# Kernel tuning notes

Hardware: AMD Instinct MI355X
Metric: run time of the kernel (lower is better)

## Reference

```python
import jax, jax.numpy as jnp
import numpy as np

MAX_GROUPS = 8
NUM_DIRECTIONS = 7
NEG = -1e9


def setup_inputs() -> dict:
    key = jax.random.key(0)
    ks = jax.random.split(key, 8)
    num_nodes, B, D = 262144, 4096, 128
    node_features = jax.random.normal(ks[0], (num_nodes, D), dtype=jnp.float32)
    global_features = jax.random.normal(ks[1], (B, D), dtype=jnp.float32)
    group_mask = jax.random.bernoulli(ks[2], 0.2, (num_nodes,))
    maneuver_valid_mask = jax.random.bernoulli(ks[3], 0.5, (B, MAX_GROUPS * NUM_DIRECTIONS))
    batch = jnp.sort(jax.random.randint(ks[4], (num_nodes,), 0, B)).astype(jnp.int32)
    w1 = jax.random.normal(ks[5], (2 * D, 128), dtype=jnp.float32) * 0.05
    b1 = jnp.zeros((128,), dtype=jnp.float32)
    w2 = jax.random.normal(ks[6], (128, NUM_DIRECTIONS), dtype=jnp.float32) * 0.05
    b2 = jnp.zeros((NUM_DIRECTIONS,), dtype=jnp.float32)
    return {"node_features": node_features, "global_features": global_features,
            "group_mask": group_mask, "maneuver_valid_mask": maneuver_valid_mask,
            "batch": batch, "w1": w1, "b1": b1, "w2": w2, "b2": b2}


def reference(node_features, global_features, group_mask, maneuver_valid_mask, batch, w1, b1, w2, b2):
    B, Dg = global_features.shape
    N, D = node_features.shape
    G, R = MAX_GROUPS, NUM_DIRECTIONS
    gm = group_mask.astype(jnp.int32)
    # batch is sorted, so within-batch group order == global node order.
    counts = jax.ops.segment_sum(gm, batch, num_segments=B)            # groups per graph
    base = jnp.concatenate([jnp.zeros((1,), jnp.int32), jnp.cumsum(counts)])[:-1]
    rank = jnp.cumsum(gm) - 1 - base[batch]                            # within-batch group index
    valid = group_mask & (rank < G)
    slot = jnp.where(valid, batch * G + rank, B * G)                   # dummy row B*G for dropped nodes
    feats = jnp.zeros((B * G + 1, D), node_features.dtype).at[slot].set(node_features)
    occ = jnp.zeros((B * G + 1,), bool).at[slot].set(valid)
    feats = feats[:-1].reshape(B, G, D)
    occ = occ[:-1].reshape(B, G)
    x = jnp.concatenate([feats, jnp.broadcast_to(global_features[:, None, :], (B, G, Dg))], axis=-1)
    h = jax.nn.relu(jnp.einsum('bgd,dk->bgk', x, w1) + b1)
    scores = jnp.einsum('bgk,kr->bgr', h, w2) + b2                     # [B, G, R]
    logits = jnp.where(occ[:, :, None], scores, NEG).reshape(B, G * R)
    return jnp.where(maneuver_valid_mask, logits, NEG)
```

## Files before the change

### kernel.cpp

```cpp
#include <hip/hip_runtime.h>


#define MAXG 8
#define NDIR 7
#define NEGV -1e9f

typedef __attribute__((ext_vector_type(8))) short s8v;
typedef __attribute__((ext_vector_type(4))) float f32x4;

__device__ inline bool readMask(const void* p, int i, int fmt) {
    switch (fmt) {
        case 0: return ((const int*)p)[i] != 0;
        case 1: return ((const unsigned char*)p)[i] != 0;
        case 2: return ((const float*)p)[i] != 0.0f;
        default: return ((const unsigned short*)p)[i] != 0;
    }
}

__global__ __launch_bounds__(256) void fused_all(
        const float* __restrict__ nf,
        const float* __restrict__ gf,
        const void*  __restrict__ gm,
        const void*  __restrict__ mv,
        const int*   __restrict__ batch,
        const float* __restrict__ w1,
        const float* __restrict__ b1,
        const float* __restrict__ w2,
        const float* __restrict__ b2,
        float* __restrict__ out,
        int N, int B)
{
    __shared__ int sStart[9];
    __shared__ int sSlot[64];
    __shared__ int sFlag[8];
    __shared__ __align__(16) short w1s[128 * 40];
    __shared__ __align__(16) float hT[64 * 132];

    int t = threadIdx.x;
    int b0 = blockIdx.x * 8;
    int rowBase = blockIdx.x * 64;

    if (t < 64) sSlot[t] = -1;
    if (t < 8)  sFlag[t] = 1;
    __syncthreads();

    {
        const unsigned int*   wg = (const unsigned int*)gm;
        const unsigned short* hg = (const unsigned short*)gm;
        const unsigned int*   wm = (const unsigned int*)mv;
        const unsigned short* hm = (const unsigned short*)mv;
        int oW=1,oH=1,oHf=1,oEv=1, pW=1,pH=1,pHf=1,pEv=1;
        for (int i = t; i < 1024; i += 256) {
            if (wg[i] > 1u) oW = 0;
            if (wm[i] > 1u) pW = 0;
        }
        for (int i = t; i < 2048; i += 256) {
            unsigned short v = hg[i];
            if (v && v != 0x3F80) oH = 0;
            if (v && v != 0x3C00) oHf = 0;
            if (!(i & 1) && v) oEv = 0;
            unsigned short u = hm[i];
            if (u && u != 0x3F80) pH = 0;
            if (u && u != 0x3C00) pHf = 0;
            if (!(i & 1) && u) pEv = 0;
        }
        if (!oW)  atomicAnd(&sFlag[0], 0);
        if (!oH)  atomicAnd(&sFlag[1], 0);
        if (!oHf) atomicAnd(&sFlag[2], 0);
        if (!oEv) atomicAnd(&sFlag[3], 0);
        if (!pW)  atomicAnd(&sFlag[4], 0);
        if (!pH)  atomicAnd(&sFlag[5], 0);
        if (!pHf) atomicAnd(&sFlag[6], 0);
        if (!pEv) atomicAnd(&sFlag[7], 0);
    }

    if (t < 9) {
        int target = b0 + t;
        int lo = 0, hi = N;
        while (lo < hi) {
            int mid = (lo + hi) >> 1;
            if (batch[mid] < target) lo = mid + 1; else hi = mid;
        }
        sStart[t] = lo;
    }
    __syncthreads();

    int fmtG, fmtM;
    if (sFlag[0]) fmtG = 0; else if (sFlag[1]) fmtG = sFlag[3] ? 2 : 3;
    else if (sFlag[2]) fmtG = 4; else fmtG = 1;
    if (sFlag[4]) fmtM = 0; else if (sFlag[5]) fmtM = sFlag[7] ? 2 : 3;
    else if (sFlag[6]) fmtM = 4; else fmtM = 1;

    int wave = t >> 6, lane = t & 63;
    for (int sub = 0; sub < 2; ++sub) {
        int lb = wave * 2 + sub;
        int s = sStart[lb], e = sStart[lb + 1];
        int count = 0;
        for (int i0 = s; i0 < e && count < MAXG; i0 += 64) {
            int i = i0 + lane;
            bool m = (i < e) && readMask(gm, i, fmtG);
            unsigned long long bal = __ballot(m);
            unsigned long long below = lane ? (bal & ((~0ULL) >> (64 - lane))) : 0ULL;
            int r = count + __popcll(below);
            if (m && r < MAXG) sSlot[lb * MAXG + r] = i;
            count += __popcll(bal);
        }
    }
    __syncthreads();

    int q = lane >> 4, c = lane & 15;
    int row = wave * 16 + c;
    int node = sSlot[row];
    int bb = b0 + (row >> 3);
    s8v aFrag[8];
#pragma unroll
    for (int ks = 0; ks < 8; ++ks) {
        bool have;
        const float* src;
        if (ks < 4) { have = (node >= 0); src = nf + ((long long)node * 128 + ks * 32 + q * 8); }
        else        { have = true;        src = gf + ((long long)bb * 128 + (ks - 4) * 32 + q * 8); }
        s8v v = {0, 0, 0, 0, 0, 0, 0, 0};
        if (have) {
            uint4 lo = *(const uint4*)src;
            uint4 hi = *(const uint4*)(src + 4);
            v = (s8v){(short)(lo.x >> 16), (short)(lo.y >> 16),
                      (short)(lo.z >> 16), (short)(lo.w >> 16),
                      (short)(hi.x >> 16), (short)(hi.y >> 16),
                      (short)(hi.z >> 16), (short)(hi.w >> 16)};
        }
        aFrag[ks] = v;
    }

    f32x4 acc[8];
#pragma unroll
    for (int nt = 0; nt < 8; ++nt) acc[nt] = (f32x4){0.f, 0.f, 0.f, 0.f};

    for (int ks = 0; ks < 8; ++ks) {
        {
            int base = t * 16;
            int kof = base >> 7;
            int n0 = base & 127;
            const float* src = w1 + ((ks * 32 + kof) * 128 + n0);
            uint4 f0 = *(const uint4*)(src);
            uint4 f1 = *(const uint4*)(src + 4);
            uint4 f2 = *(const uint4*)(src + 8);
            uint4 f3 = *(const uint4*)(src + 12);
            unsigned vals[16] = {f0.x, f0.y, f0.z, f0.w, f1.x, f1.y, f1.z, f1.w,
                                 f2.x, f2.y, f2.z, f2.w, f3.x, f3.y, f3.z, f3.w};
#pragma unroll
            for (int i = 0; i < 16; ++i)
                w1s[(n0 + i) * 40 + kof] = (short)(vals[i] >> 16);
        }
        __syncthreads();
#pragma unroll
        for (int nt = 0; nt < 8; ++nt) {
            s8v bFrag = *(const s8v*)&w1s[(nt * 16 + c) * 40 + q * 8];
            acc[nt] = __builtin_amdgcn_mfma_f32_16x16x32_bf16(aFrag[ks], bFrag, acc[nt], 0, 0, 0);
        }
        __syncthreads();
    }

#pragma unroll
    for (int nt = 0; nt < 8; ++nt) {
        int col = nt * 16 + c;
        float bv = b1[col];
#pragma unroll
        for (int reg = 0; reg < 4; ++reg) {
            int rl = wave * 16 + q * 4 + reg;
            float v = acc[nt][reg] + bv;
            hT[rl * 132 + col] = v > 0.f ? v : 0.f;
        }
    }
    __syncthreads();

    for (int tt = t; tt < 64 * NDIR; tt += 256) {
        int r2 = tt / NDIR, r = tt % NDIR;
        const float* hrow = &hT[r2 * 132];
        float s = b2[r];
#pragma unroll
        for (int k = 0; k < 128; k += 4) {
            float4 hv = *(const float4*)(hrow + k);
            s += hv.x * w2[(k + 0) * NDIR + r];
            s += hv.y * w2[(k + 1) * NDIR + r];
            s += hv.z * w2[(k + 2) * NDIR + r];
            s += hv.w * w2[(k + 3) * NDIR + r];
        }
        int gr = rowBase + r2;
        bool occ = sSlot[r2] >= 0;
        int mi = gr * NDIR + r;
        bool ok = occ && readMask(mv, mi, fmtM);
        out[mi] = ok ? s : NEGV;
    }
}

extern "C" void kernel_launch(void* const* d_in, const int* in_sizes, int n_in,
                              void* d_out, int out_size, void* d_ws, size_t ws_size,
                              hipStream_t stream) {
    const float* nf  = (const float*)d_in[0];
    const float* gf  = (const float*)d_in[1];
    const void*  gm  = d_in[2];
    const void*  mv  = d_in[3];
    const int*   bat = (const int*)d_in[4];
    const float* w1  = (const float*)d_in[5];
    const float* b1  = (const float*)d_in[6];
    const float* w2  = (const float*)d_in[7];
    const float* b2  = (const float*)d_in[8];
    float* out = (float*)d_out;

    const int N = in_sizes[4];
    const int B = in_sizes[3] / (MAXG * NDIR);

    fused_all<<<B / 8, 256, 0, stream>>>(nf, gf, gm, mv, bat,
                                         w1, b1, w2, b2, out, N, B);
}
```

Baseline: 284.5 us.

## Split fused kernel into prep, slot-assignment, and MLP kernels with pre-transposed weights

Replaces the single fused kernel with three launches. The first computes segment starts by scanning boundaries, converts w1 to a transposed bf16 copy, and detects the mask formats once. The second assigns group slots with one wave per graph. The third runs the MLP on 16 rows per block, reading B fragments directly from the global transposed weights instead of restaging w1 into LDS with syncs in every block. This removes the per-block redundant format scan, binary search, and weight conversion, at the cost of two extra launches and round trips through workspace memory.

```diff
diff --git a/kernel.cpp b/kernel.cpp
--- a/kernel.cpp
+++ b/kernel.cpp
@@ -17,33 +17,31 @@
     }
 }
 
-__global__ __launch_bounds__(256) void fused_all(
-        const float* __restrict__ nf,
-        const float* __restrict__ gf,
-        const void*  __restrict__ gm,
-        const void*  __restrict__ mv,
-        const int*   __restrict__ batch,
-        const float* __restrict__ w1,
-        const float* __restrict__ b1,
-        const float* __restrict__ w2,
-        const float* __restrict__ b2,
-        float* __restrict__ out,
-        int N, int B)
-{
-    __shared__ int sStart[9];
-    __shared__ int sSlot[64];
+__global__ __launch_bounds__(256) void prep(
+        const int* __restrict__ batch, const float* __restrict__ w1,
+        const void* __restrict__ gm, const void* __restrict__ mv,
+        int* __restrict__ fmt, int* __restrict__ start,
+        unsigned short* __restrict__ w1t, int N, int B, int sb) {
     __shared__ int sFlag[8];
-    __shared__ __align__(16) short w1s[128 * 40];
-    __shared__ __align__(16) float hT[64 * 132];
-
-    int t = threadIdx.x;
-    int b0 = blockIdx.x * 8;
-    int rowBase = blockIdx.x * 64;
-
-    if (t < 64) sSlot[t] = -1;
-    if (t < 8)  sFlag[t] = 1;
-    __syncthreads();
-
+    int blk = blockIdx.x, t = threadIdx.x;
+    if (blk < sb) {
+        int i = blk * 256 + t;
+        if (i < N) {
+            int bi = batch[i];
+            int prev = i ? batch[i - 1] : -1;
+            for (int b = prev + 1; b <= bi; ++b) start[b] = i;
+            if (i == N - 1) { for (int b = bi + 1; b <= B; ++b) start[b] = N; }
+        }
+        return;
+    }
+    int idx = (blk - sb) * 256 + t;
+    int k = idx >> 7, n = idx & 127;
+    unsigned u = __builtin_bit_cast(unsigned, w1[idx]);
+    w1t[n * 256 + k] = (unsigned short)(u >> 16);
+
+    if (blk != sb) return;
+    if (t < 8) sFlag[t] = 1;
+    __syncthreads();
     {
         const unsigned int*   wg = (const unsigned int*)gm;
         const unsigned short* hg = (const unsigned short*)gm;
@@ -59,10 +57,10 @@
             if (v && v != 0x3F80) oH = 0;
             if (v && v != 0x3C00) oHf = 0;
             if (!(i & 1) && v) oEv = 0;
-            unsigned short u = hm[i];
-            if (u && u != 0x3F80) pH = 0;
-            if (u && u != 0x3C00) pHf = 0;
-            if (!(i & 1) && u) pEv = 0;
+            unsigned short uu = hm[i];
+            if (uu && uu != 0x3F80) pH = 0;
+            if (uu && uu != 0x3C00) pHf = 0;
+            if (!(i & 1) && uu) pEv = 0;
         }
         if (!oW)  atomicAnd(&sFlag[0], 0);
         if (!oH)  atomicAnd(&sFlag[1], 0);
@@ -73,52 +71,71 @@
         if (!pHf) atomicAnd(&sFlag[6], 0);
         if (!pEv) atomicAnd(&sFlag[7], 0);
     }
-
-    if (t < 9) {
-        int target = b0 + t;
-        int lo = 0, hi = N;
-        while (lo < hi) {
-            int mid = (lo + hi) >> 1;
-            if (batch[mid] < target) lo = mid + 1; else hi = mid;
-        }
-        sStart[t] = lo;
-    }
-    __syncthreads();
-
-    int fmtG, fmtM;
-    if (sFlag[0]) fmtG = 0; else if (sFlag[1]) fmtG = sFlag[3] ? 2 : 3;
-    else if (sFlag[2]) fmtG = 4; else fmtG = 1;
-    if (sFlag[4]) fmtM = 0; else if (sFlag[5]) fmtM = sFlag[7] ? 2 : 3;
-    else if (sFlag[6]) fmtM = 4; else fmtM = 1;
+    __syncthreads();
+    if (t == 0) {
+        int fG, fM;
+        if (sFlag[0]) fG = 0; else if (sFlag[1]) fG = sFlag[3] ? 2 : 3;
+        else if (sFlag[2]) fG = 4; else fG = 1;
+        if (sFlag[4]) fM = 0; else if (sFlag[5]) fM = sFlag[7] ? 2 : 3;
+        else if (sFlag[6]) fM = 4; else fM = 1;
+        fmt[0] = fG; fmt[1] = fM;
+    }
+}
+
+__global__ __launch_bounds__(256) void slots_k(
+        const void* __restrict__ gm, const int* __restrict__ fmt,
+        const int* __restrict__ start, int* __restrict__ slot, int B) {
+    int wid  = (blockIdx.x * 256 + threadIdx.x) >> 6;
+    int lane = threadIdx.x & 63;
+    if (wid >= B) return;
+    int fmtG = fmt[0];
+    int s = start[wid], e = start[wid + 1];
+    int count = 0;
+    for (int i0 = s; i0 < e && count < MAXG; i0 += 64) {
+        int i = i0 + lane;
+        bool m = (i < e) && readMask(gm, i, fmtG);
+        unsigned long long bal = __ballot(m);
+        unsigned long long below = lane ? (bal & ((~0ULL) >> (64 - lane))) : 0ULL;
+        int r = count + __popcll(below);
+        if (m && r < MAXG) slot[wid * MAXG + r] = i;
+        count += __popcll(bal);
+    }
+    if (count > MAXG) count = MAXG;
+    if (lane >= count && lane < MAXG) slot[wid * MAXG + lane] = -1;
+}
+
+__global__ __launch_bounds__(256) void mlp(
+        const float* __restrict__ nf,
+        const float* __restrict__ gf,
+        const void*  __restrict__ mv,
+        const int*   __restrict__ fmt,
+        const int*   __restrict__ slot,
+        const unsigned short* __restrict__ w1t,
+        const float* __restrict__ b1,
+        const float* __restrict__ w2,
+        const float* __restrict__ b2,
+        float* __restrict__ out)
+{
+    __shared__ int sSlot[16];
+    __shared__ __align__(16) float hT[16 * 132];
+
+    int t = threadIdx.x, blk = blockIdx.x;
+    if (t < 16) sSlot[t] = slot[blk * 16 + t];
+    __syncthreads();
 
     int wave = t >> 6, lane = t & 63;
-    for (int sub = 0; sub < 2; ++sub) {
-        int lb = wave * 2 + sub;
-        int s = sStart[lb], e = sStart[lb + 1];
-        int count = 0;
-        for (int i0 = s; i0 < e && count < MAXG; i0 += 64) {
-            int i = i0 + lane;
-            bool m = (i < e) && readMask(gm, i, fmtG);
-            unsigned long long bal = __ballot(m);
-            unsigned long long below = lane ? (bal & ((~0ULL) >> (64 - lane))) : 0ULL;
-            int r = count + __popcll(below);
-            if (m && r < MAXG) sSlot[lb * MAXG + r] = i;
-            count += __popcll(bal);
-        }
-    }
-    __syncthreads();
-
     int q = lane >> 4, c = lane & 15;
-    int row = wave * 16 + c;
+    int row = c;
     int node = sSlot[row];
-    int bb = b0 + (row >> 3);
-    s8v aFrag[8];
+    int bgl = blk * 2 + (row >> 3);
+
+    s8v aF[8];
 #pragma unroll
     for (int ks = 0; ks < 8; ++ks) {
         bool have;
         const float* src;
         if (ks < 4) { have = (node >= 0); src = nf + ((long long)node * 128 + ks * 32 + q * 8); }
-        else        { have = true;        src = gf + ((long long)bb * 128 + (ks - 4) * 32 + q * 8); }
+        else        { have = true;        src = gf + ((long long)bgl * 128 + (ks - 4) * 32 + q * 8); }
         s8v v = {0, 0, 0, 0, 0, 0, 0, 0};
         if (have) {
             uint4 lo = *(const uint4*)src;
@@ -128,53 +145,39 @@
                       (short)(hi.x >> 16), (short)(hi.y >> 16),
                       (short)(hi.z >> 16), (short)(hi.w >> 16)};
         }
-        aFrag[ks] = v;
-    }
-
-    f32x4 acc[8];
-#pragma unroll
-    for (int nt = 0; nt < 8; ++nt) acc[nt] = (f32x4){0.f, 0.f, 0.f, 0.f};
-
+        aF[ks] = v;
+    }
+
+    int nt0 = wave * 2, nt1 = wave * 2 + 1;
+    const unsigned short* brow0 = w1t + (nt0 * 16 + c) * 256;
+    const unsigned short* brow1 = w1t + (nt1 * 16 + c) * 256;
+    f32x4 acc0 = (f32x4){0.f, 0.f, 0.f, 0.f};
+    f32x4 acc1 = (f32x4){0.f, 0.f, 0.f, 0.f};
+#pragma unroll
     for (int ks = 0; ks < 8; ++ks) {
-        {
-            int base = t * 16;
-            int kof = base >> 7;
-            int n0 = base & 127;
-            const float* src = w1 + ((ks * 32 + kof) * 128 + n0);
-            uint4 f0 = *(const uint4*)(src);
-            uint4 f1 = *(const uint4*)(src + 4);
-            uint4 f2 = *(const uint4*)(src + 8);
-            uint4 f3 = *(const uint4*)(src + 12);
-            unsigned vals[16] = {f0.x, f0.y, f0.z, f0.w, f1.x, f1.y, f1.z, f1.w,
-                                 f2.x, f2.y, f2.z, f2.w, f3.x, f3.y, f3.z, f3.w};
-#pragma unroll
-            for (int i = 0; i < 16; ++i)
-                w1s[(n0 + i) * 40 + kof] = (short)(vals[i] >> 16);
-        }
-        __syncthreads();
-#pragma unroll
-        for (int nt = 0; nt < 8; ++nt) {
-            s8v bFrag = *(const s8v*)&w1s[(nt * 16 + c) * 40 + q * 8];
-            acc[nt] = __builtin_amdgcn_mfma_f32_16x16x32_bf16(aFrag[ks], bFrag, acc[nt], 0, 0, 0);
-        }
-        __syncthreads();
-    }
-
-#pragma unroll
-    for (int nt = 0; nt < 8; ++nt) {
-        int col = nt * 16 + c;
-        float bv = b1[col];
+        int ko = ks * 32 + q * 8;
+        s8v bf0 = *(const s8v*)(brow0 + ko);
+        s8v bf1 = *(const s8v*)(brow1 + ko);
+        acc0 = __builtin_amdgcn_mfma_f32_16x16x32_bf16(aF[ks], bf0, acc0, 0, 0, 0);
+        acc1 = __builtin_amdgcn_mfma_f32_16x16x32_bf16(aF[ks], bf1, acc1, 0, 0, 0);
+    }
+
+    {
+        int col0 = nt0 * 16 + c, col1 = nt1 * 16 + c;
+        float bv0 = b1[col0], bv1 = b1[col1];
 #pragma unroll
         for (int reg = 0; reg < 4; ++reg) {
-            int rl = wave * 16 + q * 4 + reg;
-            float v = acc[nt][reg] + bv;
-            hT[rl * 132 + col] = v > 0.f ? v : 0.f;
-        }
-    }
-    __syncthreads();
-
-    for (int tt = t; tt < 64 * NDIR; tt += 256) {
-        int r2 = tt / NDIR, r = tt % NDIR;
+            int rl = q * 4 + reg;
+            float v0 = acc0[reg] + bv0;
+            float v1 = acc1[reg] + bv1;
+            hT[rl * 132 + col0] = v0 > 0.f ? v0 : 0.f;
+            hT[rl * 132 + col1] = v1 > 0.f ? v1 : 0.f;
+        }
+    }
+    __syncthreads();
+
+    if (t < 16 * NDIR) {
+        int r2 = t / NDIR, r = t % NDIR;
         const float* hrow = &hT[r2 * 132];
         float s = b2[r];
 #pragma unroll
@@ -185,22 +188,20 @@
             s += hv.z * w2[(k + 2) * NDIR + r];
             s += hv.w * w2[(k + 3) * NDIR + r];
         }
-        int gr = rowBase + r2;
-        bool occ = sSlot[r2] >= 0;
-        int mi = gr * NDIR + r;
-        bool ok = occ && readMask(mv, mi, fmtM);
-        out[mi] = ok ? s : NEGV;
+        int gr = blk * 16 + r2;
+        bool ok = (sSlot[r2] >= 0) && readMask(mv, gr * NDIR + r, fmt[1]);
+        out[gr * NDIR + r] = ok ? s : NEGV;
     }
 }
 
 extern "C" void kernel_launch(void* const* d_in, const int* in_sizes, int n_in,
                               void* d_out, int out_size, void* d_ws, size_t ws_size,
                               hipStream_t stream) {
+    const int*   bat = (const int*)d_in[4];
     const float* nf  = (const float*)d_in[0];
     const float* gf  = (const float*)d_in[1];
     const void*  gm  = d_in[2];
     const void*  mv  = d_in[3];
-    const int*   bat = (const int*)d_in[4];
     const float* w1  = (const float*)d_in[5];
     const float* b1  = (const float*)d_in[6];
     const float* w2  = (const float*)d_in[7];
@@ -210,6 +211,16 @@
     const int N = in_sizes[4];
     const int B = in_sizes[3] / (MAXG * NDIR);
 
-    fused_all<<<B / 8, 256, 0, stream>>>(nf, gf, gm, mv, bat,
-                                         w1, b1, w2, b2, out, N, B);
-}
+    char* ws = (char*)d_ws;
+    int* fmt   = (int*)(ws + 0);
+    int* start = (int*)(ws + 64);
+    size_t slotOff = 64 + (((size_t)(B + 1) * 4 + 63) / 64) * 64;
+    int* slot  = (int*)(ws + slotOff);
+    size_t w1tOff = slotOff + (size_t)B * MAXG * 4;
+    unsigned short* w1t = (unsigned short*)(ws + w1tOff);
+
+    int sb = (N + 255) / 256;
+    prep<<<sb + 128, 256, 0, stream>>>(bat, w1, gm, mv, fmt, start, w1t, N, B, sb);
+    slots_k<<<(B * 64 + 255) / 256, 256, 0, stream>>>(gm, fmt, start, slot, B);
+    mlp<<<B / 2, 256, 0, stream>>>(nf, gf, mv, fmt, slot, w1t, b1, w2, b2, out);
+}
```

New measurement: 246.6 us. -13.3%, faster.
